# Kernel tuning notes

Hardware: AMD Instinct MI355X
Metric: run time of the kernel (lower is better)

## Reference

```python
import jax, jax.numpy as jnp
import numpy as np
import math

EMBED_DIM = 512
NUM_HEADS = 8
HEAD_DIM = EMBED_DIM // NUM_HEADS
B, S = 4, 2048


def setup_inputs() -> dict:
    key = jax.random.key(0)
    ks = jax.random.split(key, 12)
    d = EMBED_DIM
    # Xavier-uniform bound for square linear layers
    bound = math.sqrt(6.0 / (d + d))
    def lin_w(k):
        return jax.random.uniform(k, (d, d), jnp.float32, -bound, bound)
    return {
        "x": jax.random.normal(ks[0], (B, S, d), jnp.float32),
        "mask": jax.random.randint(ks[1], (B, S), 0, 2) == 1,  # True = masked out
        "wq": lin_w(ks[2]), "bq": jnp.zeros((d,), jnp.float32),
        "wk": lin_w(ks[3]), "bk": jnp.zeros((d,), jnp.float32),
        "wv": lin_w(ks[4]), "bv": jnp.zeros((d,), jnp.float32),
        "wo": lin_w(ks[5]), "bo": jnp.zeros((d,), jnp.float32),
        "ln_gamma": jnp.ones((d,), jnp.float32),
        "ln_beta": jnp.zeros((d,), jnp.float32),
        "temperature": jnp.full((1,), 1.0 / math.sqrt(HEAD_DIM), jnp.float32),
    }


def _layer_norm(x, gamma, beta, eps=1e-6):
    mu = jnp.mean(x, axis=-1, keepdims=True)
    var = jnp.var(x, axis=-1, keepdims=True)
    return (x - mu) * jax.lax.rsqrt(var + eps) * gamma + beta


def reference(x, mask, wq, bq, wk, bk, wv, bv, wo, bo, ln_gamma, ln_beta, temperature):
    Bv, Sv, d = x.shape
    H, hd = NUM_HEADS, HEAD_DIM
    # torch nn.Linear: y = x @ W.T + b (W is [out, in])
    def proj(w, b):
        return (jnp.einsum("bsd,ed->bse", x, w) + b).reshape(Bv, Sv, H, hd).transpose(0, 2, 1, 3)
    q = proj(wq, bq)  # [B, H, S, hd]
    k = proj(wk, bk)
    v = proj(wv, bv)
    scores = jnp.einsum("bhqd,bhkd->bhqk", q, k) * temperature[0]  # [B,H,S,S]
    scores = jnp.where(mask[:, None, None, :], jnp.float32(-1e9), scores)
    attn = jax.nn.softmax(scores, axis=-1)  # dropout is identity in eval
    out = jnp.einsum("bhqk,bhkd->bhqd", attn, v)
    out = out.transpose(0, 2, 1, 3).reshape(Bv, Sv, d)
    out = jnp.einsum("bsd,ed->bse", out, wo) + bo
    return _layer_norm(out + x, ln_gamma, ln_beta)
```

## Files before the change

### kernel.cpp

```cpp
#include <hip/hip_runtime.h>
#include <hip/hip_bf16.h>
#include <stdint.h>

#define B_ 4
#define S_ 2048
#define D_ 512
#define H_ 8
#define HD_ 64
#define M_ (B_*S_)

typedef __bf16 bf16x8 __attribute__((ext_vector_type(8)));
typedef float f32x4 __attribute__((ext_vector_type(4)));
typedef float f32x16 __attribute__((ext_vector_type(16)));

__device__ __forceinline__ unsigned short f2b(float f) {
  union { float f; unsigned u; } v; v.f = f;
  unsigned r = v.u + 0x7fff + ((v.u >> 16) & 1);
  return (unsigned short)(r >> 16);
}

__device__ __forceinline__ float b2f(unsigned short u) {
  union { unsigned u; float f; } v; v.u = (unsigned)u << 16;
  return v.f;
}

__device__ __forceinline__ float exp2_hw(float x) {
  return __builtin_amdgcn_exp2f(x);
}

__device__ __forceinline__ unsigned cvtpk_bf16(float lo, float hi) {
  unsigned r;
  asm("v_cvt_pk_bf16_f32 %0, %1, %2" : "=v"(r) : "v"(lo), "v"(hi));
  return r;
}

__device__ __forceinline__ void plswap(unsigned &a, unsigned &b) {
  asm volatile("v_permlane32_swap_b32 %0, %1" : "+v"(a), "+v"(b));
}

__device__ __forceinline__ void gload16(const void* g, void* lds) {
  __builtin_amdgcn_global_load_lds(
      (const __attribute__((address_space(1))) unsigned int*)g,
      (__attribute__((address_space(3))) unsigned int*)lds, 16, 0, 0);
}

#define XN4 (M_ * D_ / 4)
#define WN4 (D_ * D_ / 4)
__global__ __launch_bounds__(256) void cvt_all_kernel(const float* __restrict__ x,
    const float* __restrict__ wq, const float* __restrict__ wk,
    const float* __restrict__ wv, const float* __restrict__ wo,
    unsigned short* __restrict__ xb, unsigned short* __restrict__ wqb,
    unsigned short* __restrict__ wkb, unsigned short* __restrict__ wvb,
    unsigned short* __restrict__ wob) {
  int i = blockIdx.x * blockDim.x + threadIdx.x;
  const float* src; unsigned short* dst; int off;
  if (i < XN4) { src = x; dst = xb; off = i; }
  else {
    int j = i - XN4;
    int sel = j / WN4; off = j - sel * WN4;
    src = (sel == 0) ? wq : (sel == 1) ? wk : (sel == 2) ? wv : wo;
    dst = (sel == 0) ? wqb : (sel == 1) ? wkb : (sel == 2) ? wvb : wob;
  }
  float4 v = ((const float4*)src)[off];
  ushort4 o;
  o.x = f2b(v.x); o.y = f2b(v.y); o.z = f2b(v.z); o.w = f2b(v.w);
  ((ushort4*)dst)[off] = o;
}

__global__ __launch_bounds__(64) void rank_kernel(const int* __restrict__ mask,
    int* __restrict__ idx, int* __restrict__ nkbuf) {
  int b = blockIdx.x, lane = threadIdx.x;
  const int* mb = mask + (size_t)b * S_;
  int base = 0;
  for (int c = 0; c < 32; ++c) {
    int s = c * 64 + lane;
    int m = mb[s];
    unsigned long long keep = __ballot(m == 0);
    int my = base + __popcll(keep & ((1ull << lane) - 1ull));
    if (m == 0) idx[(size_t)b * S_ + my] = s;
    base += __popcll(keep);
  }
  if (lane == 0) nkbuf[b] = base;
}

__global__ __launch_bounds__(256) void compact_kernel(const unsigned short* __restrict__ Kb,
    const unsigned short* __restrict__ Vtb, const int* __restrict__ idx,
    const int* __restrict__ nkbuf,
    unsigned short* __restrict__ Kc, unsigned short* __restrict__ Vtc) {
  int bh = blockIdx.y, b = bh >> 3;
  int nk = nkbuf[b];
  const int* ib = idx + (size_t)b * S_;
  int tid = threadIdx.x;
  if (blockIdx.z == 0) {
    int j = blockIdx.x * 32 + (tid >> 3), ch = tid & 7;
    if (j < nk) {
      int s = ib[j];
      const uint4* src = (const uint4*)&Kb[((size_t)bh * S_ + s) * HD_];
      uint4* dst = (uint4*)&Kc[((size_t)bh * S_ + j) * HD_];
      dst[ch] = src[ch];
    }
  } else {
    int d = blockIdx.x;
    const unsigned short* src = &Vtb[((size_t)bh * HD_ + d) * S_];
    unsigned short* dst = &Vtc[((size_t)bh * HD_ + d) * S_];
    int j0 = tid * 8;
    if (j0 < nk) {
      unsigned short tmp[8];
      #pragma unroll
      for (int c = 0; c < 8; ++c) {
        int j = j0 + c;
        tmp[c] = (j < nk) ? src[ib[j]] : (unsigned short)0;
      }
      *(uint4*)&dst[j0] = *(uint4*)tmp;
    }
  }
}

__device__ __forceinline__ void gemm_core_db(const unsigned short* __restrict__ A,
                                             const unsigned short* __restrict__ W,
                                             int m0, int n0, f32x4 (&acc)[4][4],
                                             unsigned short (&As)[2][128 * 64],
                                             unsigned short (&Bs)[2][128 * 64]) {
  int tid = threadIdx.x;
  int w = tid >> 6, lane = tid & 63;
  int l15 = lane & 15, g = lane >> 4;
  int wr = w >> 1, wc = w & 1;
  #define STAGE_G(buf, k0_) do {                                               \
    _Pragma("unroll")                                                          \
    for (int i = 0; i < 4; ++i) {                                              \
      int l = i * 256 + w * 64 + lane;                                         \
      int row = l >> 3, seg = l & 7;                                           \
      int sseg = seg ^ (row & 7);                                              \
      gload16(A + (size_t)(m0 + row) * D_ + (k0_) + sseg * 8,                  \
              (char*)As[buf] + (size_t)(i * 256 + w * 64) * 16);               \
      gload16(W + (size_t)(n0 + row) * D_ + (k0_) + sseg * 8,                  \
              (char*)Bs[buf] + (size_t)(i * 256 + w * 64) * 16);               \
    }                                                                          \
  } while (0)
  STAGE_G(0, 0);
  __syncthreads();
  for (int ks = 0; ks < 8; ++ks) {
    int cur = ks & 1;
    if (ks < 7) STAGE_G(cur ^ 1, (ks + 1) * 64);
    #pragma unroll
    for (int kk = 0; kk < 2; ++kk) {
      int sw = ((kk * 4 + g) ^ (l15 & 7)) * 8;
      bf16x8 af[4], bfr[4];
      #pragma unroll
      for (int t = 0; t < 4; ++t) {
        af[t]  = *(const bf16x8*)&As[cur][(wr * 64 + t * 16 + l15) * 64 + sw];
        bfr[t] = *(const bf16x8*)&Bs[cur][(wc * 64 + t * 16 + l15) * 64 + sw];
      }
      #pragma unroll
      for (int mi = 0; mi < 4; ++mi)
        #pragma unroll
        for (int ni = 0; ni < 4; ++ni)
          acc[mi][ni] = __builtin_amdgcn_mfma_f32_16x16x32_bf16(af[mi], bfr[ni], acc[mi][ni], 0, 0, 0);
    }
    __syncthreads();
  }
  #undef STAGE_G
}

__global__ __launch_bounds__(256) void gemm_qkv(const unsigned short* __restrict__ xb,
    const unsigned short* __restrict__ wqb, const unsigned short* __restrict__ wkb,
    const unsigned short* __restrict__ wvb,
    const float* __restrict__ bq, const float* __restrict__ bk, const float* __restrict__ bv,
    const float* __restrict__ tptr,
    unsigned short* __restrict__ Qb, unsigned short* __restrict__ Kb, unsigned short* __restrict__ Vtb) {
  __shared__ unsigned short As[2][128 * 64], Bs[2][128 * 64];
  int z = blockIdx.z;
  const unsigned short* W = (z == 0) ? wqb : ((z == 1) ? wkb : wvb);
  const float* bias = (z == 0) ? bq : ((z == 1) ? bk : bv);
  float scale = (z == 0) ? tptr[0] * 1.44269504088896340736f : 1.0f;
  int m0 = blockIdx.x * 128, n0 = blockIdx.y * 128;
  f32x4 zero4 = {0.f, 0.f, 0.f, 0.f};
  f32x4 acc[4][4];
  #pragma unroll
  for (int mi = 0; mi < 4; ++mi)
    #pragma unroll
    for (int ni = 0; ni < 4; ++ni) acc[mi][ni] = zero4;
  gemm_core_db(xb, W, m0, n0, acc, As, Bs);
  int tid = threadIdx.x;
  int w = tid >> 6, lane = tid & 63, l15 = lane & 15, g = lane >> 4;
  int wr = w >> 1, wc = w & 1;
  if (z == 2) {
    unsigned short* T = &As[0][0];
    #pragma unroll
    for (int mi = 0; mi < 4; ++mi)
      #pragma unroll
      for (int ni = 0; ni < 4; ++ni) {
        int el = wc * 64 + ni * 16 + l15;
        float bb = bias[n0 + el];
        int sx = (el & 15) << 3;
        #pragma unroll
        for (int r = 0; r < 4; ++r) {
          int s = wr * 64 + mi * 16 + g * 4 + r;
          T[el * 128 + (s ^ sx)] = f2b(acc[mi][ni][r] + bb);
        }
      }
    __syncthreads();
    int el = tid >> 1, hf = tid & 1;
    int eg = n0 + el, h = eg >> 6, dd = eg & 63;
    int bI = m0 >> 11, sbase = (m0 & 2047) + hf * 64;
    unsigned short* dst = &Vtb[((size_t)(bI * H_ + h) * HD_ + dd) * S_ + sbase];
    const unsigned short* srcR = &T[el * 128];
    int j = el & 15;
    #pragma unroll
    for (int c = 0; c < 8; ++c) {
      int cc = (hf * 8 + c) ^ j;
      uint4 v = *(const uint4*)&srcR[cc * 8];
      *(uint4*)&dst[c * 8] = v;
    }
  } else {
    #pragma unroll
    for (int mi = 0; mi < 4; ++mi)
      #pragma unroll
      for (int ni = 0; ni < 4; ++ni) {
        int e = n0 + wc * 64 + ni * 16 + l15;
        float bb = bias[e];
        int h = e >> 6, dd = e & 63;
        #pragma unroll
        for (int r = 0; r < 4; ++r) {
          int m = m0 + wr * 64 + mi * 16 + g * 4 + r;
          int b = m >> 11, s = m & 2047;
          unsigned short u = f2b((acc[mi][ni][r] + bb) * scale);
          int bh = b * H_ + h;
          if (z == 0) Qb[((size_t)bh * S_ + s) * HD_ + dd] = u;
          else        Kb[((size_t)bh * S_ + s) * HD_ + dd] = u;
        }
      }
  }
}

__global__ __launch_bounds__(256) void gemm_proj(const unsigned short* __restrict__ AOb,
    const unsigned short* __restrict__ wob, const float* __restrict__ bo,
    unsigned short* __restrict__ Pfb) {
  __shared__ unsigned short As[2][128 * 64], Bs[2][128 * 64];
  int m0 = blockIdx.x * 128, n0 = blockIdx.y * 128;
  f32x4 zero4 = {0.f, 0.f, 0.f, 0.f};
  f32x4 acc[4][4];
  #pragma unroll
  for (int mi = 0; mi < 4; ++mi)
    #pragma unroll
    for (int ni = 0; ni < 4; ++ni) acc[mi][ni] = zero4;
  gemm_core_db(AOb, wob, m0, n0, acc, As, Bs);
  int tid = threadIdx.x;
  int w = tid >> 6, lane = tid & 63, l15 = lane & 15, g = lane >> 4;
  int wr = w >> 1, wc = w & 1;
  #pragma unroll
  for (int mi = 0; mi < 4; ++mi)
    #pragma unroll
    for (int ni = 0; ni < 4; ++ni) {
      int e = n0 + wc * 64 + ni * 16 + l15;
      float bb = bo[e];
      #pragma unroll
      for (int r = 0; r < 4; ++r) {
        int m = m0 + wr * 64 + mi * 16 + g * 4 + r;
        Pfb[(size_t)m * D_ + e] = f2b(acc[mi][ni][r] + bb);
      }
    }
}

__global__ __launch_bounds__(256, 2) void attn_kernel(const unsigned short* __restrict__ Qb,
    const unsigned short* __restrict__ Kc, const unsigned short* __restrict__ Vtc,
    const int* __restrict__ nkbuf, unsigned short* __restrict__ AOb) {
  __shared__ unsigned short Ks[3][64 * 64], Vs[3][64 * 64];
  __shared__ uint4 mlds[32][4][2];
  int bid = blockIdx.y * gridDim.x + blockIdx.x;
  int xcd = bid & 7, jj = bid >> 3;
  int bh = xcd * 4 + (jj >> 4);
  int qblk = jj & 15;
  int b = bh >> 3, h = bh & 7;
  int tid = threadIdx.x, w = tid >> 6, lane = tid & 63;
  int l31 = lane & 31, hi = lane >> 5;
  int q0w = qblk * 128 + w * 32;
  const unsigned short* Qbase = Qb + (size_t)bh * S_ * HD_;
  int nk = nkbuf[b];
  int nt = (nk + 63) >> 6;

  bf16x8 qf[4];
  #pragma unroll
  for (int kk = 0; kk < 4; ++kk)
    qf[kk] = *(const bf16x8*)&Qbase[(size_t)(q0w + l31) * HD_ + kk * 16 + hi * 8];

  bf16x8 ones;
  #pragma unroll
  for (int c = 0; c < 8; ++c) ones[c] = (__bf16)1.0f;

  f32x16 out[2], lacc, zc;
  #pragma unroll
  for (int i = 0; i < 16; ++i) { out[0][i] = 0.f; out[1][i] = 0.f; lacc[i] = 0.f; zc[i] = 0.f; }

  f32x16 stA[2], stB[2];

  #define STAGE_KV(buf, kb_) do {                                              \
    _Pragma("unroll")                                                          \
    for (int i = 0; i < 2; ++i) {                                              \
      int l = i * 256 + w * 64 + lane;                                         \
      int row = l >> 3, seg = l & 7;                                           \
      int sseg = seg ^ (row & 7);                                              \
      gload16(Kc + ((size_t)bh * S_ + (kb_) + row) * HD_ + sseg * 8,           \
              (char*)Ks[buf] + (size_t)(i * 256 + w * 64) * 16);               \
      gload16(Vtc + ((size_t)bh * HD_ + row) * S_ + (kb_) + sseg * 8,          \
              (char*)Vs[buf] + (size_t)(i * 256 + w * 64) * 16);               \
    }                                                                          \
  } while (0)

  #define QKT_TILE(KSBUF, ST) do {                                             \
    __builtin_amdgcn_s_setprio(1);                                             \
    const unsigned short* kbase_ = Ks[KSBUF];                                  \
    _Pragma("unroll")                                                          \
    for (int kk = 0; kk < 4; ++kk) {                                           \
      int sw = ((2 * kk + hi) ^ (l31 & 7)) * 8;                                \
      bf16x8 ka0 = *(const bf16x8*)&kbase_[l31 * 64 + sw];                     \
      bf16x8 ka1 = *(const bf16x8*)&kbase_[(32 + l31) * 64 + sw];              \
      ST[0] = __builtin_amdgcn_mfma_f32_32x32x16_bf16(ka0, qf[kk], kk ? ST[0] : zc, 0, 0, 0); \
      ST[1] = __builtin_amdgcn_mfma_f32_32x32x16_bf16(ka1, qf[kk], kk ? ST[1] : zc, 0, 0, 0); \
    }                                                                          \
    __builtin_amdgcn_s_setprio(0);                                             \
  } while (0)

  #define TILE_BODY(T, STC, STN, bPV, bQK, bST) do {                           \
    __syncthreads();                                                           \
    if ((T) + 2 < nt) STAGE_KV(bST, ((T) + 2) * 64);                           \
    if ((T) + 1 < nt) QKT_TILE(bQK, STN);                                      \
    _Pragma("unroll")                                                          \
    for (int ktile = 0; ktile < 2; ++ktile)                                    \
      _Pragma("unroll")                                                        \
      for (int reg = 0; reg < 16; ++reg)                                       \
        STC[ktile][reg] = exp2_hw(STC[ktile][reg]);                            \
    __builtin_amdgcn_s_setprio(1);                                             \
    const unsigned short* vbase_ = Vs[bPV];                                    \
    _Pragma("unroll")                                                          \
    for (int kp = 0; kp < 4; ++kp) {                                           \
      const int kt8 = kp >> 1;                                                 \
      const int ro = 8 * (kp & 1);                                             \
      uint4 mw = mlds[(T)][kp][hi];                                            \
      unsigned Xa = cvtpk_bf16(STC[kt8][ro + 0], STC[kt8][ro + 1]);            \
      unsigned Ya = cvtpk_bf16(STC[kt8][ro + 4], STC[kt8][ro + 5]);            \
      unsigned Xb = cvtpk_bf16(STC[kt8][ro + 2], STC[kt8][ro + 3]);            \
      unsigned Yb = cvtpk_bf16(STC[kt8][ro + 6], STC[kt8][ro + 7]);            \
      plswap(Xa, Ya);                                                          \
      plswap(Xb, Yb);                                                          \
      union { unsigned u[4]; bf16x8 v; } pu;                                   \
      pu.u[0] = Xa & mw.x; pu.u[1] = Xb & mw.y;                                \
      pu.u[2] = Ya & mw.z; pu.u[3] = Yb & mw.w;                                \
      bf16x8 pa = pu.v;                                                        \
      _Pragma("unroll")                                                        \
      for (int dn = 0; dn < 2; ++dn) {                                         \
        int row = dn * 32 + l31;                                               \
        bf16x8 vb = *(const bf16x8*)&vbase_[row * 64 + ((2 * kp + hi) ^ (row & 7)) * 8]; \
        out[dn] = __builtin_amdgcn_mfma_f32_32x32x16_bf16(pa, vb, out[dn], 0, 0, 0); \
      }                                                                        \
      lacc = __builtin_amdgcn_mfma_f32_32x32x16_bf16(pa, ones, lacc, 0, 0, 0); \
    }                                                                          \
    __builtin_amdgcn_s_setprio(0);                                             \
  } while (0)

  STAGE_KV(0, 0);
  {
    int t = tid;
    int tile = t >> 3, kp = (t >> 1) & 3, hh = t & 1;
    int j0 = tile * 64 + kp * 16 + hh * 8;
    uint4 mw;
    mw.x = ((j0 + 0 < nk) ? 0x0000FFFFu : 0u) | ((j0 + 1 < nk) ? 0xFFFF0000u : 0u);
    mw.y = ((j0 + 2 < nk) ? 0x0000FFFFu : 0u) | ((j0 + 3 < nk) ? 0xFFFF0000u : 0u);
    mw.z = ((j0 + 4 < nk) ? 0x0000FFFFu : 0u) | ((j0 + 5 < nk) ? 0xFFFF0000u : 0u);
    mw.w = ((j0 + 6 < nk) ? 0x0000FFFFu : 0u) | ((j0 + 7 < nk) ? 0xFFFF0000u : 0u);
    mlds[tile][kp][hh] = mw;
  }
  __syncthreads();
  if (nt > 1) STAGE_KV(1, 64);
  QKT_TILE(0, stA);

  int t = 0;
  for (; t + 1 < nt; t += 2) {
    TILE_BODY(t, stA, stB, t % 3, (t + 1) % 3, (t + 2) % 3);
    TILE_BODY(t + 1, stB, stA, (t + 1) % 3, (t + 2) % 3, t % 3);
  }
  if (t < nt) TILE_BODY(t, stA, stB, t % 3, (t + 1) % 3, (t + 2) % 3);

  #pragma unroll
  for (int reg = 0; reg < 16; ++reg) {
    float inv = 1.f / lacc[reg];
    int q = q0w + (reg & 3) + 8 * (reg >> 2) + 4 * hi;
    #pragma unroll
    for (int dn = 0; dn < 2; ++dn)
      AOb[((size_t)b * S_ + q) * D_ + h * HD_ + dn * 32 + l31] = f2b(out[dn][reg] * inv);
  }
  #undef TILE_BODY
  #undef QKT_TILE
  #undef STAGE_KV
}

__global__ __launch_bounds__(256) void ln_kernel(const unsigned short* __restrict__ Pfb,
    const float* __restrict__ x, const float* __restrict__ gamma,
    const float* __restrict__ beta, float* __restrict__ out) {
  int row = blockIdx.x * 4 + (threadIdx.x >> 6);
  int lane = threadIdx.x & 63;
  const unsigned short* pr = Pfb + (size_t)row * D_;
  const float* xr = x + (size_t)row * D_;
  ushort4 p0 = *(const ushort4*)(pr + lane * 8);
  ushort4 p1 = *(const ushort4*)(pr + lane * 8 + 4);
  float4 b0 = *(const float4*)(xr + lane * 8);
  float4 b1 = *(const float4*)(xr + lane * 8 + 4);
  float y[8] = {b2f(p0.x) + b0.x, b2f(p0.y) + b0.y, b2f(p0.z) + b0.z, b2f(p0.w) + b0.w,
                b2f(p1.x) + b1.x, b2f(p1.y) + b1.y, b2f(p1.z) + b1.z, b2f(p1.w) + b1.w};
  float s = 0.f, s2 = 0.f;
  #pragma unroll
  for (int i = 0; i < 8; ++i) { s += y[i]; s2 += y[i] * y[i]; }
  #pragma unroll
  for (int d = 1; d < 64; d <<= 1) { s += __shfl_xor(s, d); s2 += __shfl_xor(s2, d); }
  float mu = s * (1.f / 512.f);
  float var = s2 * (1.f / 512.f) - mu * mu;
  float inv = rsqrtf(fmaxf(var, 0.f) + 1e-6f);
  float4 g0 = *(const float4*)(gamma + lane * 8);
  float4 g1 = *(const float4*)(gamma + lane * 8 + 4);
  float4 e0 = *(const float4*)(beta + lane * 8);
  float4 e1 = *(const float4*)(beta + lane * 8 + 4);
  float* orow = out + (size_t)row * D_;
  float4 o0 = {(y[0] - mu) * inv * g0.x + e0.x, (y[1] - mu) * inv * g0.y + e0.y,
               (y[2] - mu) * inv * g0.z + e0.z, (y[3] - mu) * inv * g0.w + e0.w};
  float4 o1 = {(y[4] - mu) * inv * g1.x + e1.x, (y[5] - mu) * inv * g1.y + e1.y,
               (y[6] - mu) * inv * g1.z + e1.z, (y[7] - mu) * inv * g1.w + e1.w};
  *(float4*)(orow + lane * 8) = o0;
  *(float4*)(orow + lane * 8 + 4) = o1;
}

extern "C" void kernel_launch(void* const* d_in, const int* in_sizes, int n_in,
                              void* d_out, int out_size, void* d_ws, size_t ws_size,
                              hipStream_t stream) {
  const float* x = (const float*)d_in[0];
  const int* mask = (const int*)d_in[1];
  const float* wq = (const float*)d_in[2];
  const float* bq = (const float*)d_in[3];
  const float* wk = (const float*)d_in[4];
  const float* bk = (const float*)d_in[5];
  const float* wv = (const float*)d_in[6];
  const float* bv = (const float*)d_in[7];
  const float* wo = (const float*)d_in[8];
  const float* bo = (const float*)d_in[9];
  const float* gamma = (const float*)d_in[10];
  const float* beta = (const float*)d_in[11];
  const float* temp = (const float*)d_in[12];
  float* out = (float*)d_out;
  char* ws = (char*)d_ws;
  const size_t MB = (size_t)1 << 20;
  unsigned short* xb  = (unsigned short*)(ws);
  unsigned short* wqb = (unsigned short*)(ws + 8 * MB);
  unsigned short* wkb = (unsigned short*)(ws + 8 * MB + 512 * 1024);
  unsigned short* wvb = (unsigned short*)(ws + 9 * MB);
  unsigned short* wob = (unsigned short*)(ws + 9 * MB + 512 * 1024);
  unsigned short* Qb  = (unsigned short*)(ws + 10 * MB);
  unsigned short* Kb  = (unsigned short*)(ws + 18 * MB);
  unsigned short* Pfb = (unsigned short*)(ws + 10 * MB);
  unsigned short* Vtb = (unsigned short*)(ws + 26 * MB);
  unsigned short* AOb = (unsigned short*)(ws + 34 * MB);
  unsigned short* Kc  = (unsigned short*)(ws + 42 * MB);
  unsigned short* Vtc = (unsigned short*)(ws + 50 * MB);
  int*            idx = (int*)(ws + 58 * MB);
  int*            nkb = (int*)(ws + 58 * MB + 64 * 1024);

  cvt_all_kernel<<<(XN4 + 4 * WN4 + 255) / 256, 256, 0, stream>>>(
      x, wq, wk, wv, wo, xb, wqb, wkb, wvb, wob);
  rank_kernel<<<4, 64, 0, stream>>>(mask, idx, nkb);
  gemm_qkv<<<dim3(64, 4, 3), 256, 0, stream>>>(xb, wqb, wkb, wvb, bq, bk, bv, temp, Qb, Kb, Vtb);
  compact_kernel<<<dim3(64, 32, 2), 256, 0, stream>>>(Kb, Vtb, idx, nkb, Kc, Vtc);
  attn_kernel<<<dim3(16, 32), 256, 0, stream>>>(Qb, Kc, Vtc, nkb, AOb);
  gemm_proj<<<dim3(64, 4), 256, 0, stream>>>(AOb, wob, bo, Pfb);
  ln_kernel<<<2048, 256, 0, stream>>>(Pfb, x, gamma, beta, out);
}
```

Before: 105.5 us.

## Fuse K compaction into QKV GEMM epilogue and use persistent grid

The rank kernel now also writes a per-position rank array, and the QKV GEMM epilogue scatters unmasked K rows straight into the compacted buffer. This removes the separate K gather pass and one full K round trip through global memory. The QKV GEMM also moves from a 3D grid of 768 blocks to 512 blocks that each take up to two tiles, which changes load balance and tile order. Pfb is moved so it no longer aliases Qb.

```diff
diff --git a/kernel.cpp b/kernel.cpp
--- a/kernel.cpp
+++ b/kernel.cpp
@@ -68,7 +68,7 @@
 }
 
 __global__ __launch_bounds__(64) void rank_kernel(const int* __restrict__ mask,
-    int* __restrict__ idx, int* __restrict__ nkbuf) {
+    int* __restrict__ idx, int* __restrict__ rank, int* __restrict__ nkbuf) {
   int b = blockIdx.x, lane = threadIdx.x;
   const int* mb = mask + (size_t)b * S_;
   int base = 0;
@@ -78,41 +78,31 @@
     unsigned long long keep = __ballot(m == 0);
     int my = base + __popcll(keep & ((1ull << lane) - 1ull));
     if (m == 0) idx[(size_t)b * S_ + my] = s;
+    rank[(size_t)b * S_ + s] = (m == 0) ? my : -1;
     base += __popcll(keep);
   }
   if (lane == 0) nkbuf[b] = base;
 }
 
-__global__ __launch_bounds__(256) void compact_kernel(const unsigned short* __restrict__ Kb,
+__global__ __launch_bounds__(256) void compact_kernel(
     const unsigned short* __restrict__ Vtb, const int* __restrict__ idx,
-    const int* __restrict__ nkbuf,
-    unsigned short* __restrict__ Kc, unsigned short* __restrict__ Vtc) {
+    const int* __restrict__ nkbuf, unsigned short* __restrict__ Vtc) {
   int bh = blockIdx.y, b = bh >> 3;
   int nk = nkbuf[b];
   const int* ib = idx + (size_t)b * S_;
   int tid = threadIdx.x;
-  if (blockIdx.z == 0) {
-    int j = blockIdx.x * 32 + (tid >> 3), ch = tid & 7;
-    if (j < nk) {
-      int s = ib[j];
-      const uint4* src = (const uint4*)&Kb[((size_t)bh * S_ + s) * HD_];
-      uint4* dst = (uint4*)&Kc[((size_t)bh * S_ + j) * HD_];
-      dst[ch] = src[ch];
+  int d = blockIdx.x;
+  const unsigned short* src = &Vtb[((size_t)bh * HD_ + d) * S_];
+  unsigned short* dst = &Vtc[((size_t)bh * HD_ + d) * S_];
+  int j0 = tid * 8;
+  if (j0 < nk) {
+    unsigned short tmp[8];
+    #pragma unroll
+    for (int c = 0; c < 8; ++c) {
+      int j = j0 + c;
+      tmp[c] = (j < nk) ? src[ib[j]] : (unsigned short)0;
     }
-  } else {
-    int d = blockIdx.x;
-    const unsigned short* src = &Vtb[((size_t)bh * HD_ + d) * S_];
-    unsigned short* dst = &Vtc[((size_t)bh * HD_ + d) * S_];
-    int j0 = tid * 8;
-    if (j0 < nk) {
-      unsigned short tmp[8];
-      #pragma unroll
-      for (int c = 0; c < 8; ++c) {
-        int j = j0 + c;
-        tmp[c] = (j < nk) ? src[ib[j]] : (unsigned short)0;
-      }
-      *(uint4*)&dst[j0] = *(uint4*)tmp;
-    }
+    *(uint4*)&dst[j0] = *(uint4*)tmp;
   }
 }
 
@@ -166,70 +156,95 @@
     const unsigned short* __restrict__ wqb, const unsigned short* __restrict__ wkb,
     const unsigned short* __restrict__ wvb,
     const float* __restrict__ bq, const float* __restrict__ bk, const float* __restrict__ bv,
-    const float* __restrict__ tptr,
-    unsigned short* __restrict__ Qb, unsigned short* __restrict__ Kb, unsigned short* __restrict__ Vtb) {
+    const float* __restrict__ tptr, const int* __restrict__ rank,
+    unsigned short* __restrict__ Qb, unsigned short* __restrict__ Kc, unsigned short* __restrict__ Vtb) {
   __shared__ unsigned short As[2][128 * 64], Bs[2][128 * 64];
-  int z = blockIdx.z;
-  const unsigned short* W = (z == 0) ? wqb : ((z == 1) ? wkb : wvb);
-  const float* bias = (z == 0) ? bq : ((z == 1) ? bk : bv);
-  float scale = (z == 0) ? tptr[0] * 1.44269504088896340736f : 1.0f;
-  int m0 = blockIdx.x * 128, n0 = blockIdx.y * 128;
-  f32x4 zero4 = {0.f, 0.f, 0.f, 0.f};
-  f32x4 acc[4][4];
-  #pragma unroll
-  for (int mi = 0; mi < 4; ++mi)
-    #pragma unroll
-    for (int ni = 0; ni < 4; ++ni) acc[mi][ni] = zero4;
-  gemm_core_db(xb, W, m0, n0, acc, As, Bs);
   int tid = threadIdx.x;
   int w = tid >> 6, lane = tid & 63, l15 = lane & 15, g = lane >> 4;
   int wr = w >> 1, wc = w & 1;
-  if (z == 2) {
-    unsigned short* T = &As[0][0];
+  #pragma unroll
+  for (int ti = 0; ti < 2; ++ti) {
+    int t = blockIdx.x + ti * 512;
+    if (t >= 768) break;
+    __syncthreads();
+    int m0 = (t / 12) * 128;
+    int nz = t % 12;
+    int z = nz >> 2;
+    int n0 = (nz & 3) * 128;
+    const unsigned short* W = (z == 0) ? wqb : ((z == 1) ? wkb : wvb);
+    const float* bias = (z == 0) ? bq : ((z == 1) ? bk : bv);
+    float scale = (z == 0) ? tptr[0] * 1.44269504088896340736f : 1.0f;
+    f32x4 zero4 = {0.f, 0.f, 0.f, 0.f};
+    f32x4 acc[4][4];
     #pragma unroll
     for (int mi = 0; mi < 4; ++mi)
       #pragma unroll
-      for (int ni = 0; ni < 4; ++ni) {
-        int el = wc * 64 + ni * 16 + l15;
-        float bb = bias[n0 + el];
-        int sx = (el & 15) << 3;
+      for (int ni = 0; ni < 4; ++ni) acc[mi][ni] = zero4;
+    gemm_core_db(xb, W, m0, n0, acc, As, Bs);
+    if (z == 2) {
+      unsigned short* T = &As[0][0];
+      #pragma unroll
+      for (int mi = 0; mi < 4; ++mi)
         #pragma unroll
-        for (int r = 0; r < 4; ++r) {
-          int s = wr * 64 + mi * 16 + g * 4 + r;
-          T[el * 128 + (s ^ sx)] = f2b(acc[mi][ni][r] + bb);
+        for (int ni = 0; ni < 4; ++ni) {
+          int el = wc * 64 + ni * 16 + l15;
+          float bb = bias[n0 + el];
+          int sx = (el & 15) << 3;
+          #pragma unroll
+          for (int r = 0; r < 4; ++r) {
+            int s = wr * 64 + mi * 16 + g * 4 + r;
+            T[el * 128 + (s ^ sx)] = f2b(acc[mi][ni][r] + bb);
+          }
         }
+      __syncthreads();
+      int el = tid >> 1, hf = tid & 1;
+      int eg = n0 + el, h = eg >> 6, dd = eg & 63;
+      int bI = m0 >> 11, sbase = (m0 & 2047) + hf * 64;
+      unsigned short* dst = &Vtb[((size_t)(bI * H_ + h) * HD_ + dd) * S_ + sbase];
+      const unsigned short* srcR = &T[el * 128];
+      int j = el & 15;
+      #pragma unroll
+      for (int c = 0; c < 8; ++c) {
+        int cc = (hf * 8 + c) ^ j;
+        uint4 v = *(const uint4*)&srcR[cc * 8];
+        *(uint4*)&dst[c * 8] = v;
       }
-    __syncthreads();
-    int el = tid >> 1, hf = tid & 1;
-    int eg = n0 + el, h = eg >> 6, dd = eg & 63;
-    int bI = m0 >> 11, sbase = (m0 & 2047) + hf * 64;
-    unsigned short* dst = &Vtb[((size_t)(bI * H_ + h) * HD_ + dd) * S_ + sbase];
-    const unsigned short* srcR = &T[el * 128];
-    int j = el & 15;
-    #pragma unroll
-    for (int c = 0; c < 8; ++c) {
-      int cc = (hf * 8 + c) ^ j;
-      uint4 v = *(const uint4*)&srcR[cc * 8];
-      *(uint4*)&dst[c * 8] = v;
+    } else if (z == 1) {
+      #pragma unroll
+      for (int mi = 0; mi < 4; ++mi)
+        #pragma unroll
+        for (int ni = 0; ni < 4; ++ni) {
+          int e = n0 + wc * 64 + ni * 16 + l15;
+          float bb = bias[e];
+          int h = e >> 6, dd = e & 63;
+          #pragma unroll
+          for (int r = 0; r < 4; ++r) {
+            int m = m0 + wr * 64 + mi * 16 + g * 4 + r;
+            int b = m >> 11, s = m & 2047;
+            int jj = rank[(size_t)b * S_ + s];
+            if (jj >= 0) {
+              unsigned short u = f2b(acc[mi][ni][r] + bb);
+              Kc[((size_t)(b * H_ + h) * S_ + jj) * HD_ + dd] = u;
+            }
+          }
+        }
+    } else {
+      #pragma unroll
+      for (int mi = 0; mi < 4; ++mi)
+        #pragma unroll
+        for (int ni = 0; ni < 4; ++ni) {
+          int e = n0 + wc * 64 + ni * 16 + l15;
+          float bb = bias[e];
+          int h = e >> 6, dd = e & 63;
+          #pragma unroll
+          for (int r = 0; r < 4; ++r) {
+            int m = m0 + wr * 64 + mi * 16 + g * 4 + r;
+            int b = m >> 11, s = m & 2047;
+            unsigned short u = f2b((acc[mi][ni][r] + bb) * scale);
+            Qb[((size_t)(b * H_ + h) * S_ + s) * HD_ + dd] = u;
+          }
+        }
     }
-  } else {
-    #pragma unroll
-    for (int mi = 0; mi < 4; ++mi)
-      #pragma unroll
-      for (int ni = 0; ni < 4; ++ni) {
-        int e = n0 + wc * 64 + ni * 16 + l15;
-        float bb = bias[e];
-        int h = e >> 6, dd = e & 63;
-        #pragma unroll
-        for (int r = 0; r < 4; ++r) {
-          int m = m0 + wr * 64 + mi * 16 + g * 4 + r;
-          int b = m >> 11, s = m & 2047;
-          unsigned short u = f2b((acc[mi][ni][r] + bb) * scale);
-          int bh = b * H_ + h;
-          if (z == 0) Qb[((size_t)bh * S_ + s) * HD_ + dd] = u;
-          else        Kb[((size_t)bh * S_ + s) * HD_ + dd] = u;
-        }
-      }
   }
 }
 
@@ -453,20 +468,20 @@
   unsigned short* wvb = (unsigned short*)(ws + 9 * MB);
   unsigned short* wob = (unsigned short*)(ws + 9 * MB + 512 * 1024);
   unsigned short* Qb  = (unsigned short*)(ws + 10 * MB);
-  unsigned short* Kb  = (unsigned short*)(ws + 18 * MB);
-  unsigned short* Pfb = (unsigned short*)(ws + 10 * MB);
+  unsigned short* Pfb = (unsigned short*)(ws + 18 * MB);
   unsigned short* Vtb = (unsigned short*)(ws + 26 * MB);
   unsigned short* AOb = (unsigned short*)(ws + 34 * MB);
   unsigned short* Kc  = (unsigned short*)(ws + 42 * MB);
   unsigned short* Vtc = (unsigned short*)(ws + 50 * MB);
   int*            idx = (int*)(ws + 58 * MB);
-  int*            nkb = (int*)(ws + 58 * MB + 64 * 1024);
+  int*            rnk = (int*)(ws + 58 * MB + 64 * 1024);
+  int*            nkb = (int*)(ws + 58 * MB + 128 * 1024);
 
   cvt_all_kernel<<<(XN4 + 4 * WN4 + 255) / 256, 256, 0, stream>>>(
       x, wq, wk, wv, wo, xb, wqb, wkb, wvb, wob);
-  rank_kernel<<<4, 64, 0, stream>>>(mask, idx, nkb);
-  gemm_qkv<<<dim3(64, 4, 3), 256, 0, stream>>>(xb, wqb, wkb, wvb, bq, bk, bv, temp, Qb, Kb, Vtb);
-  compact_kernel<<<dim3(64, 32, 2), 256, 0, stream>>>(Kb, Vtb, idx, nkb, Kc, Vtc);
+  rank_kernel<<<4, 64, 0, stream>>>(mask, idx, rnk, nkb);
+  gemm_qkv<<<512, 256, 0, stream>>>(xb, wqb, wkb, wvb, bq, bk, bv, temp, rnk, Qb, Kc, Vtb);
+  compact_kernel<<<dim3(64, 32), 256, 0, stream>>>(Vtb, idx, nkb, Vtc);
   attn_kernel<<<dim3(16, 32), 256, 0, stream>>>(Qb, Kc, Vtc, nkb, AOb);
   gemm_proj<<<dim3(64, 4), 256, 0, stream>>>(AOb, wob, bo, Pfb);
   ln_kernel<<<2048, 256, 0, stream>>>(Pfb, x, gamma, beta, out);
```

After: 103.0 us. 2.4% less time.
